# Kernel optimization log

Measured on AMD Instinct MI355X. Metric: run time of the kernel, lower is better.

## Reference

```python
import jax, jax.numpy as jnp
import numpy as np

N = 100000
IN_CH = 512
HEADS = 8
OUT_CH = 1  # forced: nn.Linear(heads, 1) consumes GAT output of size heads*out_channels
E = 3200000
NEG_SLOPE = 0.2


def setup_inputs() -> dict:
    key = jax.random.key(0)
    ks = jax.random.split(key, 8)
    x = jax.random.normal(ks[0], (N, IN_CH), dtype=jnp.float32)
    edge_index = jax.random.randint(ks[1], (2, E), 0, N, dtype=jnp.int32)
    # GATConv params
    W = jax.random.normal(ks[2], (IN_CH, HEADS * OUT_CH), dtype=jnp.float32) / np.sqrt(IN_CH)
    att_src = jax.random.normal(ks[3], (HEADS, OUT_CH), dtype=jnp.float32)
    att_dst = jax.random.normal(ks[4], (HEADS, OUT_CH), dtype=jnp.float32)
    gat_bias = jnp.zeros((HEADS * OUT_CH,), dtype=jnp.float32)
    # calibration head
    lin_w = jax.random.normal(ks[5], (1, HEADS), dtype=jnp.float32) / np.sqrt(HEADS)
    lin_b = jnp.zeros((1,), dtype=jnp.float32)
    bias = jnp.ones((1,), dtype=jnp.float32)  # init bias value 1.0
    return {"x": x, "edge_index": edge_index, "W": W, "att_src": att_src,
            "att_dst": att_dst, "gat_bias": gat_bias, "lin_w": lin_w,
            "lin_b": lin_b, "bias": bias}


def reference(x, edge_index, W, att_src, att_dst, gat_bias, lin_w, lin_b, bias):
    n = x.shape[0]
    # GATConv adds self-loops by default
    loops = jnp.arange(n, dtype=edge_index.dtype)
    src = jnp.concatenate([edge_index[0], loops])
    dst = jnp.concatenate([edge_index[1], loops])

    h = (x @ W).reshape(n, HEADS, OUT_CH)                 # [N,H,C]
    a_src = (h * att_src[None]).sum(-1)                   # [N,H]
    a_dst = (h * att_dst[None]).sum(-1)                   # [N,H]

    e = jax.nn.leaky_relu(a_src[src] + a_dst[dst], NEG_SLOPE)  # [Etot,H]
    # segment softmax over incoming edges of each dst node
    e_max = jax.ops.segment_max(e, dst, num_segments=n)        # [N,H]
    e_exp = jnp.exp(e - e_max[dst])
    denom = jax.ops.segment_sum(e_exp, dst, num_segments=n)
    alpha = e_exp / (denom[dst] + 1e-16)                       # [Etot,H]

    msg = h[src] * alpha[..., None]                            # [Etot,H,C]
    out = jax.ops.segment_sum(msg, dst, num_segments=n)        # [N,H,C]
    out = out.reshape(n, HEADS * OUT_CH) + gat_bias            # concat heads

    temperature = jax.nn.relu(out @ lin_w.T + lin_b) + bias    # [N,1]
    return temperature
```

## Files before the change

kernel.cpp:

```cpp
#include <hip/hip_runtime.h>

#define IN_CH 512
#define HEADS 8
#define NEG_SLOPE 0.2f

#define RB 256
#define RB_BITS 8
#define NB_MAX 400
#define LCAP 8
#define BCAP 9216
#define GT_STRIDE 16
#define EPT 9

__device__ __forceinline__ float lrelu(float v) {
    return v > 0.f ? v : NEG_SLOPE * v;
}

__device__ __forceinline__ void gemm_rows(const float* __restrict__ x,
                                          const float* __restrict__ W,
                                          float* __restrict__ h, int n,
                                          int wave, int nwav, int lane) {
    float4 wlo[8], whi[8];
#pragma unroll
    for (int j = 0; j < 8; ++j) {
        int k = (j < 4) ? (lane * 4 + j) : (256 + lane * 4 + (j - 4));
        const float4* p = (const float4*)(W + k * 8);
        wlo[j] = p[0];
        whi[j] = p[1];
    }
    for (int row = wave; row < n; row += nwav) {
        const float4* xr = (const float4*)(x + (size_t)row * IN_CH);
        float4 x0 = xr[lane];
        float4 x1 = xr[64 + lane];
        float xs[8] = {x0.x, x0.y, x0.z, x0.w, x1.x, x1.y, x1.z, x1.w};
        float acc[8] = {0.f, 0.f, 0.f, 0.f, 0.f, 0.f, 0.f, 0.f};
#pragma unroll
        for (int j = 0; j < 8; ++j) {
            acc[0] = fmaf(xs[j], wlo[j].x, acc[0]);
            acc[1] = fmaf(xs[j], wlo[j].y, acc[1]);
            acc[2] = fmaf(xs[j], wlo[j].z, acc[2]);
            acc[3] = fmaf(xs[j], wlo[j].w, acc[3]);
            acc[4] = fmaf(xs[j], whi[j].x, acc[4]);
            acc[5] = fmaf(xs[j], whi[j].y, acc[5]);
            acc[6] = fmaf(xs[j], whi[j].z, acc[6]);
            acc[7] = fmaf(xs[j], whi[j].w, acc[7]);
        }
#pragma unroll
        for (int off = 32; off >= 1; off >>= 1) {
#pragma unroll
            for (int hd = 0; hd < 8; ++hd)
                acc[hd] += __shfl_down(acc[hd], off, 64);
        }
        if (lane == 0) {
            float4* hp = (float4*)(h + (size_t)row * 8);
            hp[0] = make_float4(acc[0], acc[1], acc[2], acc[3]);
            hp[1] = make_float4(acc[4], acc[5], acc[6], acc[7]);
        }
    }
}

__global__ __launch_bounds__(256, 4)
void k_fused(const float* __restrict__ x, const float* __restrict__ W,
             float* __restrict__ h, const int* __restrict__ ei,
             int* __restrict__ gtail, int* __restrict__ bucket,
             int n, int E, int gemmBlocks, int nb) {
    __shared__ int lcnt[NB_MAX];
    __shared__ int gbase[NB_MAX];
    __shared__ int lst[NB_MAX * LCAP];

    if ((int)blockIdx.x < gemmBlocks) {
        const int lane = threadIdx.x & 63;
        const int wave = (int)((blockIdx.x * 256 + threadIdx.x) >> 6);
        gemm_rows(x, W, h, n, wave, gemmBlocks * 4, lane);
        return;
    }

    for (int i = threadIdx.x; i < nb; i += 256) lcnt[i] = 0;
    __syncthreads();

    int sb = blockIdx.x - gemmBlocks;
    int base = sb * 2048 + (int)threadIdx.x * 8;
    if (base < E) {
        if (base + 8 <= E) {
            int4 s0 = *(const int4*)(ei + base);
            int4 s1 = *(const int4*)(ei + base + 4);
            int4 d0 = *(const int4*)(ei + E + base);
            int4 d1 = *(const int4*)(ei + E + base + 4);
            int ss[8] = {s0.x, s0.y, s0.z, s0.w, s1.x, s1.y, s1.z, s1.w};
            int dd[8] = {d0.x, d0.y, d0.z, d0.w, d1.x, d1.y, d1.z, d1.w};
#pragma unroll
            for (int k = 0; k < 8; ++k) {
                int b = dd[k] >> RB_BITS;
                int v = (ss[k] << RB_BITS) | (dd[k] & (RB - 1));
                int p = atomicAdd(&lcnt[b], 1);
                if (p < LCAP) {
                    lst[b * LCAP + p] = v;
                } else {
                    int g = atomicAdd(gtail + (b << 4), 1);
                    if (g < BCAP) bucket[(size_t)b * BCAP + g] = v;
                }
            }
        } else {
            for (int k = 0; base + k < E; ++k) {
                int s = ei[base + k];
                int d = ei[E + base + k];
                int b = d >> RB_BITS;
                int v = (s << RB_BITS) | (d & (RB - 1));
                int p = atomicAdd(&lcnt[b], 1);
                if (p < LCAP) {
                    lst[b * LCAP + p] = v;
                } else {
                    int g = atomicAdd(gtail + (b << 4), 1);
                    if (g < BCAP) bucket[(size_t)b * BCAP + g] = v;
                }
            }
        }
    }
    __syncthreads();

    for (int b = threadIdx.x; b < nb; b += 256) {
        int c = min(lcnt[b], LCAP);
        gbase[b] = c ? atomicAdd(gtail + (b << 4), c) : 0;
    }
    __syncthreads();

    int tot = nb * LCAP;
    for (int pr = threadIdx.x; pr < tot; pr += 256) {
        int b = pr >> 3;
        int i = pr & (LCAP - 1);
        if (i < min(lcnt[b], LCAP)) {
            int pos = gbase[b] + i;
            if (pos < BCAP) bucket[(size_t)b * BCAP + pos] = lst[b * LCAP + i];
        }
    }
}

__global__ __launch_bounds__(1024, 4)
void k_agg(const float* __restrict__ h, const int* __restrict__ bucket,
           const int* __restrict__ gtail,
           const float* __restrict__ att_src, const float* __restrict__ att_dst,
           const float* __restrict__ gat_bias, const float* __restrict__ lin_w,
           const float* __restrict__ lin_b, const float* __restrict__ bias,
           float* __restrict__ out, int n) {
    __shared__ int elds[BCAP];
    __shared__ float hw[HEADS][RB];
    __shared__ int cnt[RB];
    __shared__ int scn[RB];
    __shared__ int pcnt[RB];

    const int b = blockIdx.x;
    const int base = b << RB_BITS;
    const int Wn = min(RB, n - base);
    const int tid = threadIdx.x;

    for (int i = tid; i < RB; i += 1024) { cnt[i] = 0; pcnt[i] = 0; }
    for (int i = tid; i < Wn * 8; i += 1024)
        hw[i & 7][i >> 3] = h[(size_t)(base + (i >> 3)) * 8 + (i & 7)];

    const int tail = min(gtail[b << 4], BCAP);
    const int* __restrict__ lstp = bucket + (size_t)b * BCAP;

    int vv[EPT];
#pragma unroll
    for (int r = 0; r < EPT; ++r) {
        int idx = tid + r * 1024;
        vv[r] = (idx < tail) ? lstp[idx] : -1;
    }
    __syncthreads();
#pragma unroll
    for (int r = 0; r < EPT; ++r)
        if (vv[r] >= 0) atomicAdd(&cnt[vv[r] & (RB - 1)], 1);
    __syncthreads();

    if (tid < RB) scn[tid] = cnt[tid];
    __syncthreads();
    for (int off = 1; off < RB; off <<= 1) {
        int v = 0;
        if (tid < RB) {
            v = scn[tid];
            if (tid >= off) v += scn[tid - off];
        }
        __syncthreads();
        if (tid < RB) scn[tid] = v;
        __syncthreads();
    }

#pragma unroll
    for (int r = 0; r < EPT; ++r) {
        if (vv[r] >= 0) {
            int ln = vv[r] & (RB - 1);
            int pos = scn[ln] - cnt[ln] + atomicAdd(&pcnt[ln], 1);
            if (pos < BCAP) elds[pos] = vv[r] >> RB_BITS;
        }
    }
    __syncthreads();

    float as[8], ad[8];
#pragma unroll
    for (int q = 0; q < 8; ++q) { as[q] = att_src[q]; ad[q] = att_dst[q]; }

    const int ln = tid >> 2;
    const int j = tid & 3;
    float num[8] = {0.f, 0.f, 0.f, 0.f, 0.f, 0.f, 0.f, 0.f};
    float den[8] = {0.f, 0.f, 0.f, 0.f, 0.f, 0.f, 0.f, 0.f};
    if (ln < Wn) {
        float hadd[8];
#pragma unroll
        for (int q = 0; q < 8; ++q) hadd[q] = hw[q][ln] * ad[q];
        const int deg = cnt[ln];
        const int st = scn[ln] - deg;
        int i = j;
        for (; i + 4 < deg; i += 8) {
            int s0 = elds[st + i];
            int s1 = elds[st + i + 4];
            const float4* p0 = (const float4*)(h + (size_t)s0 * 8);
            const float4* p1 = (const float4*)(h + (size_t)s1 * 8);
            float4 a0 = p0[0], b0 = p0[1];
            float4 a1 = p1[0], b1 = p1[1];
            float h0[8] = {a0.x, a0.y, a0.z, a0.w, b0.x, b0.y, b0.z, b0.w};
            float h1[8] = {a1.x, a1.y, a1.z, a1.w, b1.x, b1.y, b1.z, b1.w};
#pragma unroll
            for (int q = 0; q < 8; ++q) {
                float e0 = lrelu(fmaf(h0[q], as[q], hadd[q]));
                float p0e = __expf(e0);
                den[q] += p0e;
                num[q] = fmaf(p0e, h0[q], num[q]);
                float e1 = lrelu(fmaf(h1[q], as[q], hadd[q]));
                float p1e = __expf(e1);
                den[q] += p1e;
                num[q] = fmaf(p1e, h1[q], num[q]);
            }
        }
        for (; i < deg; i += 4) {
            int s = elds[st + i];
            const float4* hp = (const float4*)(h + (size_t)s * 8);
            float4 ha = hp[0], hb = hp[1];
            float hs[8] = {ha.x, ha.y, ha.z, ha.w, hb.x, hb.y, hb.z, hb.w};
#pragma unroll
            for (int q = 0; q < 8; ++q) {
                float e = lrelu(fmaf(hs[q], as[q], hadd[q]));
                float p = __expf(e);
                den[q] += p;
                num[q] = fmaf(p, hs[q], num[q]);
            }
        }
    }
#pragma unroll
    for (int q = 0; q < 8; ++q) {
        num[q] += __shfl_xor(num[q], 1, 64);
        num[q] += __shfl_xor(num[q], 2, 64);
        den[q] += __shfl_xor(den[q], 1, 64);
        den[q] += __shfl_xor(den[q], 2, 64);
    }

    if (ln < Wn && j == 0) {
        float t = 0.f;
        float lb = lin_b[0], bs = bias[0];
#pragma unroll
        for (int q = 0; q < 8; ++q) {
            float hv = hw[q][ln];
            float e = lrelu(hv * (as[q] + ad[q]));
            float p = __expf(e);
            float nm = fmaf(p, hv, num[q]);
            float dn = den[q] + p;
            float o = nm / (dn + 1e-16f) + gat_bias[q];
            t = fmaf(o, lin_w[q], t);
        }
        out[base + ln] = fmaxf(t + lb, 0.f) + bs;
    }
}

extern "C" void kernel_launch(void* const* d_in, const int* in_sizes, int n_in,
                              void* d_out, int out_size, void* d_ws, size_t ws_size,
                              hipStream_t stream) {
    const float* x = (const float*)d_in[0];
    const int* ei = (const int*)d_in[1];
    const float* W = (const float*)d_in[2];
    const float* att_src = (const float*)d_in[3];
    const float* att_dst = (const float*)d_in[4];
    const float* gat_bias = (const float*)d_in[5];
    const float* lin_w = (const float*)d_in[6];
    const float* lin_b = (const float*)d_in[7];
    const float* bias = (const float*)d_in[8];

    const int n = in_sizes[0] / IN_CH;
    const int E = in_sizes[1] / 2;
    const int nb = (n + RB - 1) >> RB_BITS;

    float* h = (float*)d_ws;
    int* gtail = (int*)(h + (size_t)n * HEADS);
    int* bucket = gtail + (size_t)nb * GT_STRIDE;

    hipMemsetAsync(gtail, 0, (size_t)nb * GT_STRIDE * sizeof(int), stream);

    const int GB = 1024;
    const int SB = (E + 2047) / 2048;
    k_fused<<<GB + SB, 256, 0, stream>>>(x, W, h, ei, gtail, bucket, n, E, GB, nb);
    k_agg<<<nb, 1024, 0, stream>>>(h, bucket, gtail, att_src, att_dst,
                                   gat_bias, lin_w, lin_b, bias,
                                   (float*)d_out, n);
}
```

Before: 364.5 us.

## Store per-node projections in fp16 and unroll gather loop by four

The projected features h are now written as half precision (16 bytes per node instead of 32), which halves the bytes fetched by the random per-edge gather in the aggregation kernel. The edge loop is also unrolled to four in-flight loads per thread to raise memory-level parallelism. The cost is reduced precision in h, which feeds both the attention logits and the messages, so the fp16 rounding may introduce errors beyond tolerance.

```diff
diff --git a/kernel.cpp b/kernel.cpp
--- a/kernel.cpp
+++ b/kernel.cpp
@@ -1,4 +1,5 @@
 #include <hip/hip_runtime.h>
+#include <hip/hip_fp16.h>
 
 #define IN_CH 512
 #define HEADS 8
@@ -18,7 +19,7 @@
 
 __device__ __forceinline__ void gemm_rows(const float* __restrict__ x,
                                           const float* __restrict__ W,
-                                          float* __restrict__ h, int n,
+                                          __half* __restrict__ h, int n,
                                           int wave, int nwav, int lane) {
     float4 wlo[8], whi[8];
 #pragma unroll
@@ -52,16 +53,19 @@
                 acc[hd] += __shfl_down(acc[hd], off, 64);
         }
         if (lane == 0) {
-            float4* hp = (float4*)(h + (size_t)row * 8);
-            hp[0] = make_float4(acc[0], acc[1], acc[2], acc[3]);
-            hp[1] = make_float4(acc[4], acc[5], acc[6], acc[7]);
+            __half2 o[4];
+            o[0] = __floats2half2_rn(acc[0], acc[1]);
+            o[1] = __floats2half2_rn(acc[2], acc[3]);
+            o[2] = __floats2half2_rn(acc[4], acc[5]);
+            o[3] = __floats2half2_rn(acc[6], acc[7]);
+            *(float4*)(h + (size_t)row * 8) = *(const float4*)o;
         }
     }
 }
 
 __global__ __launch_bounds__(256, 4)
 void k_fused(const float* __restrict__ x, const float* __restrict__ W,
-             float* __restrict__ h, const int* __restrict__ ei,
+             __half* __restrict__ h, const int* __restrict__ ei,
              int* __restrict__ gtail, int* __restrict__ bucket,
              int n, int E, int gemmBlocks, int nb) {
     __shared__ int lcnt[NB_MAX];
@@ -136,7 +140,7 @@
 }
 
 __global__ __launch_bounds__(1024, 4)
-void k_agg(const float* __restrict__ h, const int* __restrict__ bucket,
+void k_agg(const __half* __restrict__ h, const int* __restrict__ bucket,
            const int* __restrict__ gtail,
            const float* __restrict__ att_src, const float* __restrict__ att_dst,
            const float* __restrict__ gat_bias, const float* __restrict__ lin_w,
@@ -155,7 +159,7 @@
 
     for (int i = tid; i < RB; i += 1024) { cnt[i] = 0; pcnt[i] = 0; }
     for (int i = tid; i < Wn * 8; i += 1024)
-        hw[i & 7][i >> 3] = h[(size_t)(base + (i >> 3)) * 8 + (i & 7)];
+        hw[i & 7][i >> 3] = __half2float(h[(size_t)(base + (i >> 3)) * 8 + (i & 7)]);
 
     const int tail = min(gtail[b << 4], BCAP);
     const int* __restrict__ lstp = bucket + (size_t)b * BCAP;
@@ -210,32 +214,41 @@
         const int deg = cnt[ln];
         const int st = scn[ln] - deg;
         int i = j;
-        for (; i + 4 < deg; i += 8) {
-            int s0 = elds[st + i];
-            int s1 = elds[st + i + 4];
-            const float4* p0 = (const float4*)(h + (size_t)s0 * 8);
-            const float4* p1 = (const float4*)(h + (size_t)s1 * 8);
-            float4 a0 = p0[0], b0 = p0[1];
-            float4 a1 = p1[0], b1 = p1[1];
-            float h0[8] = {a0.x, a0.y, a0.z, a0.w, b0.x, b0.y, b0.z, b0.w};
-            float h1[8] = {a1.x, a1.y, a1.z, a1.w, b1.x, b1.y, b1.z, b1.w};
-#pragma unroll
-            for (int q = 0; q < 8; ++q) {
-                float e0 = lrelu(fmaf(h0[q], as[q], hadd[q]));
-                float p0e = __expf(e0);
-                den[q] += p0e;
-                num[q] = fmaf(p0e, h0[q], num[q]);
-                float e1 = lrelu(fmaf(h1[q], as[q], hadd[q]));
-                float p1e = __expf(e1);
-                den[q] += p1e;
-                num[q] = fmaf(p1e, h1[q], num[q]);
+        for (; i + 12 < deg; i += 16) {
+            int sv[4] = {elds[st + i], elds[st + i + 4],
+                         elds[st + i + 8], elds[st + i + 12]};
+            float4 raw[4];
+#pragma unroll
+            for (int k = 0; k < 4; ++k)
+                raw[k] = *(const float4*)(h + (size_t)sv[k] * 8);
+#pragma unroll
+            for (int k = 0; k < 4; ++k) {
+                const __half2* q2 = (const __half2*)&raw[k];
+                float2 f01 = __half22float2(q2[0]);
+                float2 f23 = __half22float2(q2[1]);
+                float2 f45 = __half22float2(q2[2]);
+                float2 f67 = __half22float2(q2[3]);
+                float hs[8] = {f01.x, f01.y, f23.x, f23.y,
+                               f45.x, f45.y, f67.x, f67.y};
+#pragma unroll
+                for (int q = 0; q < 8; ++q) {
+                    float e = lrelu(fmaf(hs[q], as[q], hadd[q]));
+                    float p = __expf(e);
+                    den[q] += p;
+                    num[q] = fmaf(p, hs[q], num[q]);
+                }
             }
         }
         for (; i < deg; i += 4) {
             int s = elds[st + i];
-            const float4* hp = (const float4*)(h + (size_t)s * 8);
-            float4 ha = hp[0], hb = hp[1];
-            float hs[8] = {ha.x, ha.y, ha.z, ha.w, hb.x, hb.y, hb.z, hb.w};
+            float4 raw = *(const float4*)(h + (size_t)s * 8);
+            const __half2* q2 = (const __half2*)&raw;
+            float2 f01 = __half22float2(q2[0]);
+            float2 f23 = __half22float2(q2[1]);
+            float2 f45 = __half22float2(q2[2]);
+            float2 f67 = __half22float2(q2[3]);
+            float hs[8] = {f01.x, f01.y, f23.x, f23.y,
+                           f45.x, f45.y, f67.x, f67.y};
 #pragma unroll
             for (int q = 0; q < 8; ++q) {
                 float e = lrelu(fmaf(hs[q], as[q], hadd[q]));
@@ -287,7 +300,7 @@
     const int E = in_sizes[1] / 2;
     const int nb = (n + RB - 1) >> RB_BITS;
 
-    float* h = (float*)d_ws;
+    __half* h = (__half*)d_ws;
     int* gtail = (int*)(h + (size_t)n * HEADS);
     int* bucket = gtail + (size_t)nb * GT_STRIDE;
 
```

After: 369.9 us. About the same (+1.5%).
